# Kernel optimization log

Hardware: AMD Instinct MI355X
Metric: run time of the kernel (lower is better)

Reference implementation:

```python
import jax, jax.numpy as jnp
import numpy as np

N = 50000      # nodes per type
E = 600000     # edges per relation
D_IN = 128
D_OUT = 64


def setup_inputs() -> dict:
    key = jax.random.key(0)
    ks = jax.random.split(key, 12)
    x_v0 = jax.random.normal(ks[0], (N, D_IN), dtype=jnp.float32)
    x_v1 = jax.random.normal(ks[1], (N, D_IN), dtype=jnp.float32)
    edge_v0 = jax.random.randint(ks[2], (2, E), 0, N, dtype=jnp.int64)
    edge_v1 = jax.random.randint(ks[3], (2, E), 0, N, dtype=jnp.int64)
    s = 1.0 / np.sqrt(D_IN)
    Wrel0 = jax.random.uniform(ks[4], (D_OUT, D_IN), jnp.float32, -s, s)
    brel0 = jax.random.uniform(ks[5], (D_OUT,), jnp.float32, -s, s)
    Wroot0 = jax.random.uniform(ks[6], (D_OUT, D_IN), jnp.float32, -s, s)
    Wrel1 = jax.random.uniform(ks[7], (D_OUT, D_IN), jnp.float32, -s, s)
    brel1 = jax.random.uniform(ks[8], (D_OUT,), jnp.float32, -s, s)
    Wroot1 = jax.random.uniform(ks[9], (D_OUT, D_IN), jnp.float32, -s, s)
    sf = 1.0 / np.sqrt(2 * D_OUT)
    Wfc = jax.random.uniform(ks[10], (1, 2 * D_OUT), jnp.float32, -sf, sf)
    bfc = jax.random.uniform(ks[11], (1,), jnp.float32, -sf, sf)
    return {"x_v0": x_v0, "x_v1": x_v1, "edge_v0": edge_v0, "edge_v1": edge_v1,
            "Wrel0": Wrel0, "brel0": brel0, "Wroot0": Wroot0,
            "Wrel1": Wrel1, "brel1": brel1, "Wroot1": Wroot1,
            "Wfc": Wfc, "bfc": bfc}


def _graph_conv(x, edge_index, Wrel, brel, Wroot):
    # PyG GraphConv (aggr='add'): out = lin_rel(sum_{j in N(i)} x_j) + lin_root(x_i)
    src, dst = edge_index[0], edge_index[1]
    agg = jax.ops.segment_sum(x[src], dst, num_segments=x.shape[0])  # [N, D_IN]
    return agg @ Wrel.T + brel + x @ Wroot.T


def reference(x_v0, x_v1, edge_v0, edge_v1, Wrel0, brel0, Wroot0,
              Wrel1, brel1, Wroot1, Wfc, bfc):
    h0 = jax.nn.relu(_graph_conv(x_v0, edge_v0, Wrel0, brel0, Wroot0))  # [N, 64]
    h1 = jax.nn.relu(_graph_conv(x_v1, edge_v1, Wrel1, brel1, Wroot1))  # [N, 64]
    h = jnp.concatenate([h0, h1], axis=1)  # [N, 128]
    return h @ Wfc.T + bfc  # [N, 1]
```

## Files before the change

### kernel.cpp

```cpp
#include <hip/hip_runtime.h>
#include <hip/hip_bf16.h>

typedef __attribute__((ext_vector_type(8))) short short8;
typedef __attribute__((ext_vector_type(4))) float floatx4;

#define NB    1000
#define BPN   50
#define BCAP  832
#define CHUNK 2048
#define NPASS 293

static __device__ __forceinline__ unsigned short bf16_of(float f) {
    union { float f; unsigned u; } v; v.f = f;
    unsigned r = (v.u + 0x7FFF + ((v.u >> 16) & 1)) >> 16;
    return (unsigned short)r;
}
static __device__ __forceinline__ float lo_f(unsigned u) {
    union { float f; unsigned u; } v; v.u = u << 16; return v.f;
}
static __device__ __forceinline__ float hi_f(unsigned u) {
    union { float f; unsigned u; } v; v.u = u & 0xFFFF0000u; return v.f;
}

__global__ __launch_bounds__(256) void convert_w(
    const float* __restrict__ Wrel0, const float* __restrict__ Wroot0,
    const float* __restrict__ Wrel1, const float* __restrict__ Wroot1,
    unsigned short* __restrict__ Wb0, unsigned short* __restrict__ Wb1,
    int* __restrict__ cur0, int* __restrict__ cur1)
{
    int c = blockIdx.x * 256 + threadIdx.x;
    if (c < NB)          cur0[c] = 0;
    else if (c < 2 * NB) cur1[c - NB] = 0;
    if (c >= 4096) return;

    const float* s; unsigned short* d;
    if      (c < 1024) { s = Wrel0 + c * 8;           d = Wb0 + c * 8; }
    else if (c < 2048) { int t = c - 1024; s = Wroot0 + t * 8; d = Wb0 + 8192 + t * 8; }
    else if (c < 3072) { int t = c - 2048; s = Wrel1 + t * 8;  d = Wb1 + t * 8; }
    else               { int t = c - 3072; s = Wroot1 + t * 8; d = Wb1 + 8192 + t * 8; }

    floatx4 v0 = *(const floatx4*)s;
    floatx4 v1 = *(const floatx4*)(s + 4);
    short8 r = { (short)bf16_of(v0[0]), (short)bf16_of(v0[1]),
                 (short)bf16_of(v0[2]), (short)bf16_of(v0[3]),
                 (short)bf16_of(v1[0]), (short)bf16_of(v1[1]),
                 (short)bf16_of(v1[2]), (short)bf16_of(v1[3]) };
    *(short8*)d = r;
}

union SmemU {
    struct { short x_sh[32 * 136]; short w_sh[128 * 136]; } g;
    struct {
        unsigned int   stage[CHUNK];
        unsigned short sbuck[CHUNK];
        int hist[NB]; int loff[NB]; int lcur[NB]; int gbase[NB];
        int scanb[256];
    } p;
};

__global__ __launch_bounds__(256) void gemm_and_pass(
    const float* __restrict__ X0, const float* __restrict__ X1,
    const unsigned short* __restrict__ Wb0, const unsigned short* __restrict__ Wb1,
    unsigned short* __restrict__ Yrel0, unsigned short* __restrict__ Yrel1,
    unsigned short* __restrict__ Yroot0, unsigned short* __restrict__ Yroot1,
    const int* __restrict__ e0, const int* __restrict__ e1,
    unsigned int* __restrict__ pairs0, unsigned int* __restrict__ pairs1,
    int* __restrict__ cur0, int* __restrict__ cur1, int E, int N)
{
    __shared__ __align__(16) SmemU sm;
    const int tid = threadIdx.x;
    const int rel = blockIdx.y;

    if (blockIdx.x < NPASS) {
        const int* e        = rel ? e1 : e0;
        unsigned int* pairs = rel ? pairs1 : pairs0;
        int* cur            = rel ? cur1 : cur0;

        const int c0 = blockIdx.x * CHUNK;
        const int n  = min(CHUNK, E - c0);

        for (int b = tid; b < NB; b += 256) sm.p.hist[b] = 0;
        __syncthreads();

        int dsts[CHUNK / 256];
#pragma unroll
        for (int k = 0; k < CHUNK / 256; ++k) {
            int i = c0 + k * 256 + tid;
            int dst = (i < c0 + n) ? e[E + i] : -1;
            dsts[k] = dst;
            if ((unsigned)dst < (unsigned)N)
                atomicAdd(&sm.p.hist[(unsigned)dst / BPN], 1);
        }
        __syncthreads();

        int t4 = tid * 4, v[4], s = 0;
#pragma unroll
        for (int k = 0; k < 4; ++k) {
            int b = t4 + k;
            v[k] = (b < NB) ? sm.p.hist[b] : 0;
            s += v[k];
        }
        sm.p.scanb[tid] = s;
        __syncthreads();
        for (int off = 1; off < 256; off <<= 1) {
            int x = (tid >= off) ? sm.p.scanb[tid - off] : 0;
            __syncthreads();
            sm.p.scanb[tid] += x;
            __syncthreads();
        }
        int run = sm.p.scanb[tid] - s;
#pragma unroll
        for (int k = 0; k < 4; ++k) {
            int b = t4 + k;
            if (b < NB) { sm.p.loff[b] = run; sm.p.lcur[b] = run; }
            run += v[k];
        }
        for (int b = tid; b < NB; b += 256)
            sm.p.gbase[b] = (sm.p.hist[b] > 0) ? atomicAdd(&cur[b], sm.p.hist[b]) : 0;
        __syncthreads();

#pragma unroll
        for (int k = 0; k < CHUNK / 256; ++k) {
            int i   = c0 + k * 256 + tid;
            int dst = dsts[k];
            if ((unsigned)dst < (unsigned)N) {
                int src = e[i];
                unsigned usrc = ((unsigned)src < (unsigned)N) ? (unsigned)src : 0u;
                int b = (unsigned)dst / BPN;
                int p = atomicAdd(&sm.p.lcur[b], 1);
                sm.p.stage[p] = ((unsigned)dst << 16) | usrc;
                sm.p.sbuck[p] = (unsigned short)b;
            }
        }
        __syncthreads();

        int total = sm.p.scanb[255];
        for (int p = tid; p < total; p += 256) {
            int b = sm.p.sbuck[p];
            int g = sm.p.gbase[b] + (p - sm.p.loff[b]);
            if (g < BCAP)
                pairs[(size_t)b * BCAP + g] = sm.p.stage[p];
        }
        return;
    }

    const float* X           = rel ? X1 : X0;
    const unsigned short* Wb = rel ? Wb1 : Wb0;
    unsigned short* Yrel     = rel ? Yrel1 : Yrel0;
    unsigned short* Yroot    = rel ? Yroot1 : Yroot0;

    const int m0 = (blockIdx.x - NPASS) * 32;

#pragma unroll
    for (int i = 0; i < 8; ++i) {
        int c   = tid + 256 * i;
        int row = c >> 4;
        int kc  = (c & 15) * 8;
        *(short8*)&sm.g.w_sh[row * 136 + kc] = *(const short8*)(Wb + row * 128 + kc);
    }
#pragma unroll
    for (int i = 0; i < 4; ++i) {
        int c    = tid + 256 * i;
        int row  = c >> 5;
        int f    = (c & 31) * 4;
        int node = m0 + row;
        floatx4 v = {};
        if (node < N) v = *(const floatx4*)(X + (size_t)node * 128 + f);
        short* d = &sm.g.x_sh[row * 136 + f];
        d[0] = (short)bf16_of(v[0]); d[1] = (short)bf16_of(v[1]);
        d[2] = (short)bf16_of(v[2]); d[3] = (short)bf16_of(v[3]);
    }
    __syncthreads();

    const int w    = tid >> 6;
    const int lane = tid & 63;
    const int q    = lane >> 4;
    const int r    = lane & 15;

    floatx4 acc[2][2] = {};
#pragma unroll
    for (int ko = 0; ko < 4; ++ko) {
        int kb = ko * 32 + q * 8;
        short8 a0 = *(const short8*)&sm.g.x_sh[(r) * 136 + kb];
        short8 a1 = *(const short8*)&sm.g.x_sh[(16 + r) * 136 + kb];
        short8 b0 = *(const short8*)&sm.g.w_sh[(w * 32 + r) * 136 + kb];
        short8 b1 = *(const short8*)&sm.g.w_sh[(w * 32 + 16 + r) * 136 + kb];
        acc[0][0] = __builtin_amdgcn_mfma_f32_16x16x32_bf16(a0, b0, acc[0][0], 0, 0, 0);
        acc[0][1] = __builtin_amdgcn_mfma_f32_16x16x32_bf16(a0, b1, acc[0][1], 0, 0, 0);
        acc[1][0] = __builtin_amdgcn_mfma_f32_16x16x32_bf16(a1, b0, acc[1][0], 0, 0, 0);
        acc[1][1] = __builtin_amdgcn_mfma_f32_16x16x32_bf16(a1, b1, acc[1][1], 0, 0, 0);
    }

#pragma unroll
    for (int mt = 0; mt < 2; ++mt)
#pragma unroll
        for (int nt = 0; nt < 2; ++nt) {
            int col = w * 32 + nt * 16 + r;
#pragma unroll
            for (int reg = 0; reg < 4; ++reg) {
                int node = m0 + mt * 16 + q * 4 + reg;
                if (node < N) {
                    if (col < 64) Yrel[(size_t)node * 64 + col] = bf16_of(acc[mt][nt][reg]);
                    else          Yroot[(size_t)node * 64 + (col - 64)] = bf16_of(acc[mt][nt][reg]);
                }
            }
        }
}

__global__ __launch_bounds__(512) void bucket_gather(
    const unsigned int* __restrict__ pairs0, const unsigned int* __restrict__ pairs1,
    const int* __restrict__ cur0, const int* __restrict__ cur1,
    const unsigned short* __restrict__ Yrel0, const unsigned short* __restrict__ Yrel1,
    const unsigned short* __restrict__ Yroot0, const unsigned short* __restrict__ Yroot1,
    const float* __restrict__ brel0, const float* __restrict__ brel1,
    const float* __restrict__ wfc, const float* __restrict__ bfc,
    float* __restrict__ out, int N)
{
    __shared__ unsigned short slist0[BCAP], slist1[BCAP];
    __shared__ int cnt0s[BPN], cnt1s[BPN];
    __shared__ int off0s[BPN], off1s[BPN];
    __shared__ int cur0s[BPN], cur1s[BPN];

    const int tid  = threadIdx.x;
    const int b    = blockIdx.x;
    const int wv   = tid >> 6;
    const int lane = tid & 63;
    const int c    = lane & 31;
    const int half = lane >> 5;

    for (int i = tid; i < BPN; i += 512) { cnt0s[i] = 0; cnt1s[i] = 0; }
    __syncthreads();

    const int n0 = min(cur0[b], BCAP);
    const int n1 = min(cur1[b], BCAP);
    const unsigned base = (unsigned)(b * BPN);

    for (int j = tid; j < n0; j += 512)
        atomicAdd(&cnt0s[(pairs0[(size_t)b * BCAP + j] >> 16) - base], 1);
    for (int j = tid; j < n1; j += 512)
        atomicAdd(&cnt1s[(pairs1[(size_t)b * BCAP + j] >> 16) - base], 1);
    __syncthreads();

    if (wv == 0) {
        int cc = (lane < BPN) ? cnt0s[lane] : 0;
        int inc = cc;
#pragma unroll
        for (int d = 1; d < 64; d <<= 1) {
            int t = __shfl_up(inc, d, 64);
            if (lane >= d) inc += t;
        }
        if (lane < BPN) { off0s[lane] = inc - cc; cur0s[lane] = inc - cc; }
    } else if (wv == 1) {
        int cc = (lane < BPN) ? cnt1s[lane] : 0;
        int inc = cc;
#pragma unroll
        for (int d = 1; d < 64; d <<= 1) {
            int t = __shfl_up(inc, d, 64);
            if (lane >= d) inc += t;
        }
        if (lane < BPN) { off1s[lane] = inc - cc; cur1s[lane] = inc - cc; }
    }
    __syncthreads();

    for (int j = tid; j < n0; j += 512) {
        unsigned p = pairs0[(size_t)b * BCAP + j];
        int pos = atomicAdd(&cur0s[(p >> 16) - base], 1);
        slist0[pos] = (unsigned short)(p & 0xFFFFu);
    }
    for (int j = tid; j < n1; j += 512) {
        unsigned p = pairs1[(size_t)b * BCAP + j];
        int pos = atomicAdd(&cur1s[(p >> 16) - base], 1);
        slist1[pos] = (unsigned short)(p & 0xFFFFu);
    }
    __syncthreads();

    const float2 br0 = ((const float2*)brel0)[c];
    const float2 br1 = ((const float2*)brel1)[c];
    const float2 w0  = ((const float2*)wfc)[c];
    const float2 w1  = ((const float2*)(wfc + 64))[c];
    const float bias = bfc[0];

    for (int nl = wv; nl < BPN; nl += 8) {
        int i = b * BPN + nl;
        float a0x = 0.f, a0y = 0.f, a1x = 0.f, a1y = 0.f;

        {
            int st = off0s[nl], d = cnt0s[nl], j = 0;
            for (; j + 7 < d; j += 8) {
                int i0 = slist0[st + j + half];
                int i1 = slist0[st + j + 2 + half];
                int i2 = slist0[st + j + 4 + half];
                int i3 = slist0[st + j + 6 + half];
                unsigned u0 = ((const unsigned*)(Yrel0 + ((size_t)i0 << 6)))[c];
                unsigned u1 = ((const unsigned*)(Yrel0 + ((size_t)i1 << 6)))[c];
                unsigned u2 = ((const unsigned*)(Yrel0 + ((size_t)i2 << 6)))[c];
                unsigned u3 = ((const unsigned*)(Yrel0 + ((size_t)i3 << 6)))[c];
                a0x += (lo_f(u0) + lo_f(u1)) + (lo_f(u2) + lo_f(u3));
                a0y += (hi_f(u0) + hi_f(u1)) + (hi_f(u2) + hi_f(u3));
            }
            for (; j < d; j += 2) {
                int jj = j + half;
                int idx = slist0[st + (jj < d ? jj : d - 1)];
                unsigned u = ((const unsigned*)(Yrel0 + ((size_t)idx << 6)))[c];
                if (jj < d) { a0x += lo_f(u); a0y += hi_f(u); }
            }
        }
        {
            int st = off1s[nl], d = cnt1s[nl], j = 0;
            for (; j + 7 < d; j += 8) {
                int i0 = slist1[st + j + half];
                int i1 = slist1[st + j + 2 + half];
                int i2 = slist1[st + j + 4 + half];
                int i3 = slist1[st + j + 6 + half];
                unsigned u0 = ((const unsigned*)(Yrel1 + ((size_t)i0 << 6)))[c];
                unsigned u1 = ((const unsigned*)(Yrel1 + ((size_t)i1 << 6)))[c];
                unsigned u2 = ((const unsigned*)(Yrel1 + ((size_t)i2 << 6)))[c];
                unsigned u3 = ((const unsigned*)(Yrel1 + ((size_t)i3 << 6)))[c];
                a1x += (lo_f(u0) + lo_f(u1)) + (lo_f(u2) + lo_f(u3));
                a1y += (hi_f(u0) + hi_f(u1)) + (hi_f(u2) + hi_f(u3));
            }
            for (; j < d; j += 2) {
                int jj = j + half;
                int idx = slist1[st + (jj < d ? jj : d - 1)];
                unsigned u = ((const unsigned*)(Yrel1 + ((size_t)idx << 6)))[c];
                if (jj < d) { a1x += lo_f(u); a1y += hi_f(u); }
            }
        }

        a0x += __shfl_xor(a0x, 32, 64);
        a0y += __shfl_xor(a0y, 32, 64);
        a1x += __shfl_xor(a1x, 32, 64);
        a1y += __shfl_xor(a1y, 32, 64);

        unsigned ur0 = ((const unsigned*)(Yroot0 + ((size_t)i << 6)))[c];
        unsigned ur1 = ((const unsigned*)(Yroot1 + ((size_t)i << 6)))[c];

        float h0x = fmaxf(a0x + br0.x + lo_f(ur0), 0.f);
        float h0y = fmaxf(a0y + br0.y + hi_f(ur0), 0.f);
        float h1x = fmaxf(a1x + br1.x + lo_f(ur1), 0.f);
        float h1y = fmaxf(a1y + br1.y + hi_f(ur1), 0.f);
        float s = h0x * w0.x + h0y * w0.y + h1x * w1.x + h1y * w1.y;

#pragma unroll
        for (int m = 16; m > 0; m >>= 1) s += __shfl_xor(s, m, 64);
        if (lane == 0) out[i] = s + bias;
    }
}

extern "C" void kernel_launch(void* const* d_in, const int* in_sizes, int n_in,
                              void* d_out, int out_size, void* d_ws, size_t ws_size,
                              hipStream_t stream)
{
    const int N = in_sizes[0] / 128;
    const int E = in_sizes[2] / 2;

    const float* x0     = (const float*)d_in[0];
    const float* x1     = (const float*)d_in[1];
    const int*   e0     = (const int*)d_in[2];
    const int*   e1     = (const int*)d_in[3];
    const float* Wrel0  = (const float*)d_in[4];
    const float* brel0  = (const float*)d_in[5];
    const float* Wroot0 = (const float*)d_in[6];
    const float* Wrel1  = (const float*)d_in[7];
    const float* brel1  = (const float*)d_in[8];
    const float* Wroot1 = (const float*)d_in[9];
    const float* wfc    = (const float*)d_in[10];
    const float* bfc    = (const float*)d_in[11];
    float* out = (float*)d_out;

    unsigned short* Wb0   = (unsigned short*)d_ws;
    unsigned short* Wb1   = Wb0 + 128 * 128;
    unsigned short* Yrel0 = Wb1 + 128 * 128;
    unsigned short* Yrel1 = Yrel0 + (size_t)N * 64;
    unsigned short* Yroot0 = Yrel1 + (size_t)N * 64;
    unsigned short* Yroot1 = Yroot0 + (size_t)N * 64;
    unsigned int* pairs0 = (unsigned int*)(Yroot1 + (size_t)N * 64);
    unsigned int* pairs1 = pairs0 + (size_t)NB * BCAP;
    int* cur0 = (int*)(pairs1 + (size_t)NB * BCAP);
    int* cur1 = cur0 + NB;

    convert_w<<<16, 256, 0, stream>>>(Wrel0, Wroot0, Wrel1, Wroot1,
                                      Wb0, Wb1, cur0, cur1);

    const int gemm_nblk = (N + 31) / 32;
    dim3 fused_grid(NPASS + gemm_nblk, 2);
    gemm_and_pass<<<fused_grid, 256, 0, stream>>>(
        x0, x1, Wb0, Wb1, Yrel0, Yrel1, Yroot0, Yroot1,
        e0, e1, pairs0, pairs1, cur0, cur1, E, N);

    bucket_gather<<<NB, 512, 0, stream>>>(pairs0, pairs1, cur0, cur1,
                                          Yrel0, Yrel1, Yroot0, Yroot1,
                                          brel0, brel1, wfc, bfc, out, N);
}
```

Measured before the change: 175.0 us.

## Keep GEMM weights in registers, double row tile, use wave-shuffle scan

The GEMM blocks now load their bf16 weight fragments straight from global memory into registers rather than staging the full 128x128 weight tile in shared memory. Each block covers 64 rows instead of 32, which halves the number of GEMM blocks and the repeated weight loads, and the shared-memory footprint drops. The partition pass's block-wide prefix scan is replaced by a wavefront shuffle scan plus a small cross-wave combine, removing many barriers. Register pressure rises from holding eight weight fragments and eight accumulators per thread, and X conversion stores are vectorised.

New measurement: 167.8 us. -4.1%, faster.

```diff
diff --git a/kernel.cpp b/kernel.cpp
--- a/kernel.cpp
+++ b/kernel.cpp
@@ -2,6 +2,7 @@
 #include <hip/hip_bf16.h>
 
 typedef __attribute__((ext_vector_type(8))) short short8;
+typedef __attribute__((ext_vector_type(4))) short short4v;
 typedef __attribute__((ext_vector_type(4))) float floatx4;
 
 #define NB    1000
@@ -9,6 +10,7 @@
 #define BCAP  832
 #define CHUNK 2048
 #define NPASS 293
+#define BM    64
 
 static __device__ __forceinline__ unsigned short bf16_of(float f) {
     union { float f; unsigned u; } v; v.f = f;
@@ -49,12 +51,12 @@
 }
 
 union SmemU {
-    struct { short x_sh[32 * 136]; short w_sh[128 * 136]; } g;
+    struct { short x_sh[BM * 136]; } g;
     struct {
         unsigned int   stage[CHUNK];
         unsigned short sbuck[CHUNK];
         int hist[NB]; int loff[NB]; int lcur[NB]; int gbase[NB];
-        int scanb[256];
+        int scanb[8];
     } p;
 };
 
@@ -100,15 +102,24 @@
             v[k] = (b < NB) ? sm.p.hist[b] : 0;
             s += v[k];
         }
-        sm.p.scanb[tid] = s;
+        const int lane6 = tid & 63;
+        const int wv6   = tid >> 6;
+        int inc = s;
+#pragma unroll
+        for (int d = 1; d < 64; d <<= 1) {
+            int t = __shfl_up(inc, d, 64);
+            if (lane6 >= d) inc += t;
+        }
+        if (lane6 == 63) sm.p.scanb[wv6] = inc;
         __syncthreads();
-        for (int off = 1; off < 256; off <<= 1) {
-            int x = (tid >= off) ? sm.p.scanb[tid - off] : 0;
-            __syncthreads();
-            sm.p.scanb[tid] += x;
-            __syncthreads();
-        }
-        int run = sm.p.scanb[tid] - s;
+        int wo = 0, total = 0;
+#pragma unroll
+        for (int k = 0; k < 4; ++k) {
+            int ws = sm.p.scanb[k];
+            if (k < wv6) wo += ws;
+            total += ws;
+        }
+        int run = wo + inc - s;
 #pragma unroll
         for (int k = 0; k < 4; ++k) {
             int b = t4 + k;
@@ -134,7 +145,6 @@
         }
         __syncthreads();
 
-        int total = sm.p.scanb[255];
         for (int p = tid; p < total; p += 256) {
             int b = sm.p.sbuck[p];
             int g = sm.p.gbase[b] + (p - sm.p.loff[b]);
@@ -149,60 +159,59 @@
     unsigned short* Yrel     = rel ? Yrel1 : Yrel0;
     unsigned short* Yroot    = rel ? Yroot1 : Yroot0;
 
-    const int m0 = (blockIdx.x - NPASS) * 32;
+    const int m0   = (blockIdx.x - NPASS) * BM;
+    const int w    = tid >> 6;
+    const int lane = tid & 63;
+    const int q    = lane >> 4;
+    const int r    = lane & 15;
+
+    short8 bw[2][4];
+#pragma unroll
+    for (int nt = 0; nt < 2; ++nt)
+#pragma unroll
+        for (int ko = 0; ko < 4; ++ko)
+            bw[nt][ko] = *(const short8*)(Wb + (w * 32 + nt * 16 + r) * 128 + ko * 32 + q * 8);
 
 #pragma unroll
     for (int i = 0; i < 8; ++i) {
-        int c   = tid + 256 * i;
-        int row = c >> 4;
-        int kc  = (c & 15) * 8;
-        *(short8*)&sm.g.w_sh[row * 136 + kc] = *(const short8*)(Wb + row * 128 + kc);
-    }
-#pragma unroll
-    for (int i = 0; i < 4; ++i) {
         int c    = tid + 256 * i;
         int row  = c >> 5;
         int f    = (c & 31) * 4;
         int node = m0 + row;
         floatx4 v = {};
         if (node < N) v = *(const floatx4*)(X + (size_t)node * 128 + f);
-        short* d = &sm.g.x_sh[row * 136 + f];
-        d[0] = (short)bf16_of(v[0]); d[1] = (short)bf16_of(v[1]);
-        d[2] = (short)bf16_of(v[2]); d[3] = (short)bf16_of(v[3]);
+        short4v sv = { (short)bf16_of(v[0]), (short)bf16_of(v[1]),
+                       (short)bf16_of(v[2]), (short)bf16_of(v[3]) };
+        *(short4v*)&sm.g.x_sh[row * 136 + f] = sv;
     }
     __syncthreads();
 
-    const int w    = tid >> 6;
-    const int lane = tid & 63;
-    const int q    = lane >> 4;
-    const int r    = lane & 15;
-
-    floatx4 acc[2][2] = {};
+    floatx4 acc[4][2] = {};
 #pragma unroll
     for (int ko = 0; ko < 4; ++ko) {
         int kb = ko * 32 + q * 8;
-        short8 a0 = *(const short8*)&sm.g.x_sh[(r) * 136 + kb];
-        short8 a1 = *(const short8*)&sm.g.x_sh[(16 + r) * 136 + kb];
-        short8 b0 = *(const short8*)&sm.g.w_sh[(w * 32 + r) * 136 + kb];
-        short8 b1 = *(const short8*)&sm.g.w_sh[(w * 32 + 16 + r) * 136 + kb];
-        acc[0][0] = __builtin_amdgcn_mfma_f32_16x16x32_bf16(a0, b0, acc[0][0], 0, 0, 0);
-        acc[0][1] = __builtin_amdgcn_mfma_f32_16x16x32_bf16(a0, b1, acc[0][1], 0, 0, 0);
-        acc[1][0] = __builtin_amdgcn_mfma_f32_16x16x32_bf16(a1, b0, acc[1][0], 0, 0, 0);
-        acc[1][1] = __builtin_amdgcn_mfma_f32_16x16x32_bf16(a1, b1, acc[1][1], 0, 0, 0);
-    }
-
-#pragma unroll
-    for (int mt = 0; mt < 2; ++mt)
+        short8 a[4];
+#pragma unroll
+        for (int mt = 0; mt < 4; ++mt)
+            a[mt] = *(const short8*)&sm.g.x_sh[(mt * 16 + r) * 136 + kb];
+#pragma unroll
+        for (int mt = 0; mt < 4; ++mt) {
+            acc[mt][0] = __builtin_amdgcn_mfma_f32_16x16x32_bf16(a[mt], bw[0][ko], acc[mt][0], 0, 0, 0);
+            acc[mt][1] = __builtin_amdgcn_mfma_f32_16x16x32_bf16(a[mt], bw[1][ko], acc[mt][1], 0, 0, 0);
+        }
+    }
+
+    unsigned short* Yp = (w < 2) ? Yrel : Yroot;
+    const int cbase = (w & 1) * 32;
+#pragma unroll
+    for (int mt = 0; mt < 4; ++mt)
 #pragma unroll
         for (int nt = 0; nt < 2; ++nt) {
-            int col = w * 32 + nt * 16 + r;
+            int col = cbase + nt * 16 + r;
 #pragma unroll
             for (int reg = 0; reg < 4; ++reg) {
                 int node = m0 + mt * 16 + q * 4 + reg;
-                if (node < N) {
-                    if (col < 64) Yrel[(size_t)node * 64 + col] = bf16_of(acc[mt][nt][reg]);
-                    else          Yroot[(size_t)node * 64 + (col - 64)] = bf16_of(acc[mt][nt][reg]);
-                }
+                if (node < N) Yp[(size_t)node * 64 + col] = bf16_of(acc[mt][nt][reg]);
             }
         }
 }
@@ -382,7 +391,7 @@
     convert_w<<<16, 256, 0, stream>>>(Wrel0, Wroot0, Wrel1, Wroot1,
                                       Wb0, Wb1, cur0, cur1);
 
-    const int gemm_nblk = (N + 31) / 32;
+    const int gemm_nblk = (N + BM - 1) / BM;
     dim3 fused_grid(NPASS + gemm_nblk, 2);
     gemm_and_pass<<<fused_grid, 256, 0, stream>>>(
         x0, x1, Wb0, Wb1, Yrel0, Yrel1, Yroot0, Yroot1,
```
